# Performance work log

Hardware: AMD Instinct MI355X
Metric: run time of the kernel (lower is better)

The kernel has to match this reference:

```python
import jax, jax.numpy as jnp
import numpy as np

N_HEADS = 16
N_KV_HEADS = 4
ROPE_BASE = 10000.0


def rotate_half(x):
    d = x.shape[-1] // 2
    return jnp.concatenate((-x[..., d:], x[..., :d]), axis=-1)


def rope_cos_sin(seq_len, head_dim, dtype):
    inv_freq = 1.0 / (ROPE_BASE ** (jnp.arange(0, head_dim, 2, dtype=jnp.float32) / head_dim))
    t = jnp.arange(seq_len, dtype=jnp.float32)
    freqs = jnp.outer(t, inv_freq)            # [S, d/2]
    emb = jnp.concatenate((freqs, freqs), axis=-1)  # [S, d]
    return emb.astype(dtype), None  # placeholder; cos/sin computed by caller


def setup_inputs() -> dict:
    key = jax.random.key(0)
    ks = jax.random.split(key, 5)
    B, S, H = 1, 2048, 2048
    kv_dim = (H // N_HEADS) * N_KV_HEADS  # 512
    scale = 1.0 / np.sqrt(H)
    return {
        "hidden_states": jax.random.normal(ks[0], (B, S, H), dtype=jnp.float32),
        "Wq": jax.random.normal(ks[1], (H, H), dtype=jnp.float32) * scale,
        "Wk": jax.random.normal(ks[2], (kv_dim, H), dtype=jnp.float32) * scale,
        "Wv": jax.random.normal(ks[3], (kv_dim, H), dtype=jnp.float32) * scale,
        "Wo": jax.random.normal(ks[4], (H, H), dtype=jnp.float32) * scale,
    }


def reference(hidden_states, Wq, Wk, Wv, Wo):
    B, S, H = hidden_states.shape
    nH, nKV = N_HEADS, N_KV_HEADS
    d = H // nH
    groups = nH // nKV

    # projections (nn.Linear: y = x @ W.T)
    q = (hidden_states @ Wq.T).reshape(B, S, nH, d)   # [B,S,nH,d]
    k = (hidden_states @ Wk.T).reshape(B, S, nKV, d)  # [B,S,nKV,d]
    v = (hidden_states @ Wv.T).reshape(B, S, nKV, d)

    # RoPE
    inv_freq = 1.0 / (ROPE_BASE ** (jnp.arange(0, d, 2, dtype=jnp.float32) / d))
    freqs = jnp.outer(jnp.arange(S, dtype=jnp.float32), inv_freq)  # [S,d/2]
    emb = jnp.concatenate((freqs, freqs), axis=-1)                 # [S,d]
    cos = jnp.cos(emb)[None, :, None, :]
    sin = jnp.sin(emb)[None, :, None, :]
    q = q * cos + rotate_half(q) * sin
    k = k * cos + rotate_half(k) * sin

    # GQA: repeat_interleave kv heads over head axis
    k = jnp.repeat(k, groups, axis=2)  # [B,S,nH,d]
    v = jnp.repeat(v, groups, axis=2)

    # causal scaled dot-product attention
    scores = jnp.einsum('bqhd,bkhd->bhqk', q, k) / jnp.sqrt(jnp.asarray(d, q.dtype))
    causal = jnp.tril(jnp.ones((S, S), dtype=bool))
    scores = jnp.where(causal[None, None], scores, jnp.asarray(-jnp.inf, scores.dtype))
    probs = jax.nn.softmax(scores, axis=-1)
    out = jnp.einsum('bhqk,bkhd->bqhd', probs, v)  # [B,S,nH,d]
    out = out.reshape(B, S, H) @ Wo.T
    return out
```

## Files before the change

kernel.cpp:

```cpp
#include <hip/hip_runtime.h>
#include <cstdint>
#include <cstddef>


typedef __bf16 bf16_t;
typedef bf16_t bf16x4_t __attribute__((ext_vector_type(4)));
typedef bf16_t bf16x8_t __attribute__((ext_vector_type(8)));
typedef float f32x4_t __attribute__((ext_vector_type(4)));

__device__ __forceinline__ void async_copy16(void* lds_base, const void* gsrc) {
  auto g = reinterpret_cast<__attribute__((address_space(1))) void*>(
      reinterpret_cast<uintptr_t>(gsrc));
  auto l = reinterpret_cast<__attribute__((address_space(3))) void*>(
      static_cast<uint32_t>(reinterpret_cast<uintptr_t>(lds_base)));
  __builtin_amdgcn_global_load_lds(g, l, 16, 0, 0);
}

__global__ __launch_bounds__(256) void cvt_all(const float* __restrict__ hs,
                                               const float* __restrict__ wq,
                                               const float* __restrict__ wk,
                                               const float* __restrict__ wv,
                                               const float* __restrict__ wo,
                                               bf16_t* __restrict__ regA,
                                               bf16_t* __restrict__ regB,
                                               bf16_t* __restrict__ regWo) {
  const int b = blockIdx.x;
  const float* src;
  bf16_t* dst;
  int rel;
  if (b < 4096) { src = hs; dst = regA; rel = b; }
  else if (b < 8192) { src = wq; dst = regB; rel = b - 4096; }
  else if (b < 9216) { src = wk; dst = regB + 4194304; rel = b - 8192; }
  else if (b < 10240) { src = wv; dst = regB + 5242880; rel = b - 9216; }
  else { src = wo; dst = regWo; rel = b - 10240; }
  const int i = (rel * 256 + threadIdx.x) * 4;
  float4 v = *(const float4*)(src + i);
  bf16x4_t o = {(bf16_t)v.x, (bf16_t)v.y, (bf16_t)v.z, (bf16_t)v.w};
  *(bf16x4_t*)(dst + i) = o;
}

template <typename OutT, bool ROPE>
__global__ __launch_bounds__(256) void gemm_bt64(const bf16_t* __restrict__ A,
                                                 const bf16_t* __restrict__ B,
                                                 OutT* __restrict__ C,
                                                 int M, int N, int K) {
  __shared__ bf16_t As[64 * 64];
  __shared__ bf16_t Bs[128 * 64];
  const int tid = threadIdx.x;
  const int lane = tid & 63;
  const int quad = lane >> 4;
  const int l15 = lane & 15;
  const int l7 = l15 & 7;
  const int wave = tid >> 6;
  const int bm = blockIdx.x * 64;
  const int bn = blockIdx.y * 128;
  const int wm = (wave >> 1) * 32;
  const int wn32 = (wave & 1) * 32;
  const int coff[4] = {wn32, wn32 + 16, wn32 + 64, wn32 + 80};

  f32x4_t acc[2][4] = {};

  for (int k0 = 0; k0 < K; k0 += 64) {
#pragma unroll
    for (int it = 0; it < 2; ++it) {
      const int slot = it * 256 + tid;
      const int r = slot >> 3;
      const int q = (slot & 7) ^ (r & 7);
      const int wbase = it * 2048 + (tid & 192) * 8;
      async_copy16(As + wbase, A + (size_t)(bm + r) * K + k0 + q * 8);
    }
#pragma unroll
    for (int it = 0; it < 4; ++it) {
      const int slot = it * 256 + tid;
      const int r = slot >> 3;
      const int q = (slot & 7) ^ (r & 7);
      const int wbase = it * 2048 + (tid & 192) * 8;
      async_copy16(Bs + wbase, B + (size_t)(bn + r) * K + k0 + q * 8);
    }
    __syncthreads();
#pragma unroll
    for (int kk = 0; kk < 64; kk += 32) {
      const int kc = kk >> 3;
      bf16x8_t af[2], bfv[4];
#pragma unroll
      for (int i = 0; i < 2; ++i)
        af[i] = *(const bf16x8_t*)(As + (wm + i * 16 + l15) * 64 +
                                   (((kc + quad) ^ l7) * 8));
#pragma unroll
      for (int i = 0; i < 4; ++i)
        bfv[i] = *(const bf16x8_t*)(Bs + (coff[i] + l15) * 64 +
                                    (((kc + quad) ^ l7) * 8));
#pragma unroll
      for (int mi = 0; mi < 2; ++mi)
#pragma unroll
        for (int ni = 0; ni < 4; ++ni)
          acc[mi][ni] = __builtin_amdgcn_mfma_f32_16x16x32_bf16(
              af[mi], bfv[ni], acc[mi][ni], 0, 0, 0);
    }
    __syncthreads();
  }

  if (ROPE && bn < 2560) {
#pragma unroll
    for (int pair = 0; pair < 2; ++pair) {
      const int i_d = wn32 + pair * 16 + l15;
      const float inv = exp2f(-(float)i_d * 0.20762050593045702f);
#pragma unroll
      for (int mi = 0; mi < 2; ++mi) {
#pragma unroll
        for (int r = 0; r < 4; ++r) {
          const int s_row = bm + wm + mi * 16 + quad * 4 + r;
          float sn, cs;
          sincosf((float)s_row * inv, &sn, &cs);
          const float x0 = acc[mi][pair][r];
          const float x1 = acc[mi][pair + 2][r];
          acc[mi][pair][r] = x0 * cs - x1 * sn;
          acc[mi][pair + 2][r] = x1 * cs + x0 * sn;
        }
      }
    }
  }

#pragma unroll
  for (int mi = 0; mi < 2; ++mi) {
#pragma unroll
    for (int r = 0; r < 4; ++r) {
      const int row = bm + wm + mi * 16 + quad * 4 + r;
#pragma unroll
      for (int ni = 0; ni < 4; ++ni)
        C[(size_t)row * N + bn + coff[ni] + l15] = (OutT)acc[mi][ni][r];
    }
  }
}

__global__ __launch_bounds__(256) void attn_kernel(
    const bf16_t* __restrict__ qkv, float* __restrict__ Op,
    float* __restrict__ lp) {
  __shared__ bf16_t Ks[64 * 128];
  __shared__ bf16_t Vt[128 * 64];
  __shared__ bf16_t Ps[4 * 16 * 64];
  const int tid = threadIdx.x;
  const int lane = tid & 63;
  const int wave = tid >> 6;
  const int quad = lane >> 4;
  const int l15 = lane & 15;
  const int l7 = l15 & 7;
  const int j = blockIdx.x;
  const int half = j >> 9;
  const int j2 = j & 511;
  const int qb = (j2 < 256) ? (31 - (j2 >> 4)) : ((j2 - 256) >> 4);
  const int h = j2 & 15;
  const int kvh = h >> 2;
  const int nh0 = (qb + 2) >> 1;
  const int kbS = half ? nh0 : 0;
  const int kbE = half ? (qb + 1) : nh0;
  const float scale = 0.08838834764831845f;

  const int rk0 = tid >> 4;
  const int cq = tid & 15;
  const int dv2 = lane * 2;

  bf16x8_t qf[4];
  {
    const bf16_t* qbase =
        qkv + (size_t)(qb * 64 + wave * 16 + l15) * 3072 + h * 128 + quad * 8;
#pragma unroll
    for (int kf = 0; kf < 4; ++kf) qf[kf] = *(const bf16x8_t*)(qbase + kf * 32);
  }

  f32x4_t o[8] = {};
  float lsum[4] = {0.f, 0.f, 0.f, 0.f};

  bf16x8_t kreg[4];
  uint32_t vbuf[2][8];
  auto load_tile = [&](int kb) {
    const bf16_t* kbase = qkv + (size_t)(kb * 64) * 3072 + 2048 + kvh * 128;
    const bf16_t* vbase = qkv + (size_t)(kb * 64) * 3072 + 2560 + kvh * 128;
#pragma unroll
    for (int it = 0; it < 4; ++it)
      kreg[it] =
          *(const bf16x8_t*)(kbase + (size_t)(it * 16 + rk0) * 3072 + cq * 8);
#pragma unroll
    for (int it = 0; it < 2; ++it) {
      const int kg8 = it * 4 + wave;
#pragma unroll
      for (int t = 0; t < 8; ++t)
        vbuf[it][t] =
            *(const uint32_t*)(vbase + (size_t)(kg8 * 8 + t) * 3072 + dv2);
    }
  };

  if (kbS < kbE) {
    load_tile(kbS);

    for (int kb = kbS; kb < kbE; ++kb) {
      __syncthreads();
#pragma unroll
      for (int it = 0; it < 4; ++it)
        *(bf16x8_t*)(Ks + (it * 16 + rk0) * 128 + ((cq ^ rk0) * 8)) = kreg[it];
#pragma unroll
      for (int it = 0; it < 2; ++it) {
        const int kg8 = it * 4 + wave;
        bf16x8_t lov, hiv;
#pragma unroll
        for (int t = 0; t < 8; ++t) {
          const uint32_t u = vbuf[it][t];
          lov[t] = __builtin_bit_cast(bf16_t, (unsigned short)(u & 0xffff));
          hiv[t] = __builtin_bit_cast(bf16_t, (unsigned short)(u >> 16));
        }
        *(bf16x8_t*)(Vt + (size_t)dv2 * 64 + ((kg8 ^ (dv2 & 7)) * 8)) = lov;
        *(bf16x8_t*)(Vt + (size_t)(dv2 + 1) * 64 +
                     ((kg8 ^ ((dv2 + 1) & 7)) * 8)) = hiv;
      }
      __syncthreads();
      if (kb + 1 < kbE) load_tile(kb + 1);

      f32x4_t sc[4] = {};
#pragma unroll
      for (int kf = 0; kf < 4; ++kf) {
#pragma unroll
        for (int ni = 0; ni < 4; ++ni) {
          bf16x8_t bfr = *(const bf16x8_t*)(Ks + (ni * 16 + l15) * 128 +
                                            (((kf * 4 + quad) ^ l15) * 8));
          sc[ni] = __builtin_amdgcn_mfma_f32_16x16x32_bf16(qf[kf], bfr, sc[ni],
                                                           0, 0, 0);
        }
      }

      float p[4][4];
#pragma unroll
      for (int r = 0; r < 4; ++r) {
        const int sq = qb * 64 + wave * 16 + quad * 4 + r;
#pragma unroll
        for (int ni = 0; ni < 4; ++ni) {
          float arg = fmaf(sc[ni][r], scale, -16.0f);
          if (kb == qb && (kb * 64 + ni * 16 + l15) > sq) arg = -100.0f;
          const float e = __expf(arg);
          p[ni][r] = e;
          lsum[r] += e;
        }
      }

      bf16_t* pw = Ps + wave * 16 * 64;
#pragma unroll
      for (int ni = 0; ni < 4; ++ni)
#pragma unroll
        for (int r = 0; r < 4; ++r) {
          const int prow = quad * 4 + r;
          pw[prow * 64 + (((ni * 2 + (l15 >> 3)) ^ (prow & 7)) * 8) + l7] =
              (bf16_t)p[ni][r];
        }

#pragma unroll
      for (int kf = 0; kf < 2; ++kf) {
        bf16x8_t af =
            *(const bf16x8_t*)(pw + l15 * 64 + (((kf * 4 + quad) ^ l7) * 8));
#pragma unroll
        for (int ni = 0; ni < 8; ++ni) {
          bf16x8_t bfr = *(const bf16x8_t*)(Vt + (ni * 16 + l15) * 64 +
                                            (((kf * 4 + quad) ^ l7) * 8));
          o[ni] =
              __builtin_amdgcn_mfma_f32_16x16x32_bf16(af, bfr, o[ni], 0, 0, 0);
        }
      }
    }
  }

#pragma unroll
  for (int m = 1; m <= 8; m <<= 1)
#pragma unroll
    for (int r = 0; r < 4; ++r) lsum[r] += __shfl_xor(lsum[r], m, 64);

  float* obase = Op + (size_t)half * 4194304 +
                 (size_t)(qb * 64 + wave * 16 + quad * 4) * 2048 + h * 128 + l15;
#pragma unroll
  for (int r = 0; r < 4; ++r) {
#pragma unroll
    for (int ni = 0; ni < 8; ++ni)
      obase[(size_t)r * 2048 + ni * 16] = o[ni][r];
    if (l15 == 0) {
      const int row = qb * 64 + wave * 16 + quad * 4 + r;
      lp[(half * 2048 + row) * 16 + h] = lsum[r];
    }
  }
}

__global__ __launch_bounds__(256) void combine_kernel(
    const float* __restrict__ Op, const float* __restrict__ lp,
    bf16_t* __restrict__ out) {
  const int idx = (blockIdx.x * 256 + threadIdx.x) * 4;
  const int s = idx >> 11;
  const int col = idx & 2047;
  const int h = col >> 7;
  const float l = lp[s * 16 + h] + lp[(2048 + s) * 16 + h];
  const float inv = 1.0f / l;
  float4 a = *(const float4*)(Op + (size_t)s * 2048 + col);
  float4 b = *(const float4*)(Op + 4194304 + (size_t)s * 2048 + col);
  bf16x4_t o = {(bf16_t)((a.x + b.x) * inv), (bf16_t)((a.y + b.y) * inv),
                (bf16_t)((a.z + b.z) * inv), (bf16_t)((a.w + b.w) * inv)};
  *(bf16x4_t*)(out + idx) = o;
}

extern "C" void kernel_launch(void* const* d_in, const int* in_sizes, int n_in,
                              void* d_out, int out_size, void* d_ws, size_t ws_size,
                              hipStream_t stream) {
  const float* hidden = (const float*)d_in[0];
  const float* Wq = (const float*)d_in[1];
  const float* Wk = (const float*)d_in[2];
  const float* Wv = (const float*)d_in[3];
  const float* Wo = (const float*)d_in[4];

  char* ws = (char*)d_ws;
  bf16_t* regA = (bf16_t*)ws;
  bf16_t* regB = (bf16_t*)(ws + (size_t)(8u << 20));
  float* Opart = (float*)(ws + (size_t)(8u << 20));
  bf16_t* regC = (bf16_t*)(ws + (size_t)(40u << 20));
  bf16_t* regWo = (bf16_t*)(ws + (size_t)(53u << 20));
  float* lpart = (float*)(ws + (size_t)(61u << 20));

  cvt_all<<<14336, 256, 0, stream>>>(hidden, Wq, Wk, Wv, Wo, regA, regB, regWo);

  gemm_bt64<bf16_t, true><<<dim3(32, 24), 256, 0, stream>>>(regA, regB, regC,
                                                            2048, 3072, 2048);

  attn_kernel<<<1024, 256, 0, stream>>>(regC, Opart, lpart);

  combine_kernel<<<4096, 256, 0, stream>>>(Opart, lpart, regA);

  gemm_bt64<float, false><<<dim3(32, 16), 256, 0, stream>>>(
      regA, regWo, (float*)d_out, 2048, 2048, 2048);
}
```

Measured before the change: 217.4 us.

## Double attention query tile per block to reuse K/V tiles across two row groups

Each attention block now handles 128 query rows (32 per wave, as two 16-row MFMA groups) instead of 64, so every K/V tile loaded into LDS feeds twice as many MFMAs. The grid drops from 1024 to 512 blocks, and the causal split into two halves is recomputed over 64-wide key tiles with a new mask condition. This cuts global K/V traffic and LDS staging per unit of work, at the cost of more registers per thread (doubled accumulators and Q fragments), a larger P buffer, and fewer blocks to keep the GPU occupied.

```diff
diff --git a/kernel.cpp b/kernel.cpp
--- a/kernel.cpp
+++ b/kernel.cpp
@@ -138,7 +138,7 @@
     float* __restrict__ lp) {
   __shared__ bf16_t Ks[64 * 128];
   __shared__ bf16_t Vt[128 * 64];
-  __shared__ bf16_t Ps[4 * 16 * 64];
+  __shared__ bf16_t Ps[4 * 32 * 64];
   const int tid = threadIdx.x;
   const int lane = tid & 63;
   const int wave = tid >> 6;
@@ -146,30 +146,32 @@
   const int l15 = lane & 15;
   const int l7 = l15 & 7;
   const int j = blockIdx.x;
-  const int half = j >> 9;
-  const int j2 = j & 511;
-  const int qb = (j2 < 256) ? (31 - (j2 >> 4)) : ((j2 - 256) >> 4);
-  const int h = j2 & 15;
+  const int half = (j >= 256);
+  const int qb = half ? ((j - 256) >> 4) : (15 - (j >> 4));
+  const int h = j & 15;
   const int kvh = h >> 2;
-  const int nh0 = (qb + 2) >> 1;
-  const int kbS = half ? nh0 : 0;
-  const int kbE = half ? (qb + 1) : nh0;
+  const int nt = 2 * qb + 2;
+  const int kbS = half ? (qb + 1) : 0;
+  const int kbE = half ? nt : (qb + 1);
   const float scale = 0.08838834764831845f;
 
   const int rk0 = tid >> 4;
   const int cq = tid & 15;
   const int dv2 = lane * 2;
 
-  bf16x8_t qf[4];
-  {
+  bf16x8_t qf[2][4];
+#pragma unroll
+  for (int g = 0; g < 2; ++g) {
     const bf16_t* qbase =
-        qkv + (size_t)(qb * 64 + wave * 16 + l15) * 3072 + h * 128 + quad * 8;
-#pragma unroll
-    for (int kf = 0; kf < 4; ++kf) qf[kf] = *(const bf16x8_t*)(qbase + kf * 32);
-  }
-
-  f32x4_t o[8] = {};
-  float lsum[4] = {0.f, 0.f, 0.f, 0.f};
+        qkv + (size_t)(qb * 128 + wave * 32 + g * 16 + l15) * 3072 + h * 128 +
+        quad * 8;
+#pragma unroll
+    for (int kf = 0; kf < 4; ++kf)
+      qf[g][kf] = *(const bf16x8_t*)(qbase + kf * 32);
+  }
+
+  f32x4_t o[2][8] = {};
+  float lsum[2][4] = {};
 
   bf16x8_t kreg[4];
   uint32_t vbuf[2][8];
@@ -190,78 +192,87 @@
     }
   };
 
-  if (kbS < kbE) {
-    load_tile(kbS);
-
-    for (int kb = kbS; kb < kbE; ++kb) {
-      __syncthreads();
-#pragma unroll
-      for (int it = 0; it < 4; ++it)
-        *(bf16x8_t*)(Ks + (it * 16 + rk0) * 128 + ((cq ^ rk0) * 8)) = kreg[it];
-#pragma unroll
-      for (int it = 0; it < 2; ++it) {
-        const int kg8 = it * 4 + wave;
-        bf16x8_t lov, hiv;
-#pragma unroll
-        for (int t = 0; t < 8; ++t) {
-          const uint32_t u = vbuf[it][t];
-          lov[t] = __builtin_bit_cast(bf16_t, (unsigned short)(u & 0xffff));
-          hiv[t] = __builtin_bit_cast(bf16_t, (unsigned short)(u >> 16));
-        }
-        *(bf16x8_t*)(Vt + (size_t)dv2 * 64 + ((kg8 ^ (dv2 & 7)) * 8)) = lov;
-        *(bf16x8_t*)(Vt + (size_t)(dv2 + 1) * 64 +
-                     ((kg8 ^ ((dv2 + 1) & 7)) * 8)) = hiv;
-      }
-      __syncthreads();
-      if (kb + 1 < kbE) load_tile(kb + 1);
-
-      f32x4_t sc[4] = {};
-#pragma unroll
-      for (int kf = 0; kf < 4; ++kf) {
+  load_tile(kbS);
+
+  for (int kb = kbS; kb < kbE; ++kb) {
+    __syncthreads();
+#pragma unroll
+    for (int it = 0; it < 4; ++it)
+      *(bf16x8_t*)(Ks + (it * 16 + rk0) * 128 + ((cq ^ rk0) * 8)) = kreg[it];
+#pragma unroll
+    for (int it = 0; it < 2; ++it) {
+      const int kg8 = it * 4 + wave;
+      bf16x8_t lov, hiv;
+#pragma unroll
+      for (int t = 0; t < 8; ++t) {
+        const uint32_t u = vbuf[it][t];
+        lov[t] = __builtin_bit_cast(bf16_t, (unsigned short)(u & 0xffff));
+        hiv[t] = __builtin_bit_cast(bf16_t, (unsigned short)(u >> 16));
+      }
+      *(bf16x8_t*)(Vt + (size_t)dv2 * 64 + ((kg8 ^ (dv2 & 7)) * 8)) = lov;
+      *(bf16x8_t*)(Vt + (size_t)(dv2 + 1) * 64 +
+                   ((kg8 ^ ((dv2 + 1) & 7)) * 8)) = hiv;
+    }
+    __syncthreads();
+    if (kb + 1 < kbE) load_tile(kb + 1);
+
+    f32x4_t sc[2][4] = {};
+#pragma unroll
+    for (int kf = 0; kf < 4; ++kf) {
+#pragma unroll
+      for (int ni = 0; ni < 4; ++ni) {
+        bf16x8_t bfr = *(const bf16x8_t*)(Ks + (ni * 16 + l15) * 128 +
+                                          (((kf * 4 + quad) ^ l15) * 8));
+#pragma unroll
+        for (int g = 0; g < 2; ++g)
+          sc[g][ni] = __builtin_amdgcn_mfma_f32_16x16x32_bf16(
+              qf[g][kf], bfr, sc[g][ni], 0, 0, 0);
+      }
+    }
+
+    const bool need_mask = (kb >= 2 * qb);
+#pragma unroll
+    for (int g = 0; g < 2; ++g) {
+      float p[4][4];
+#pragma unroll
+      for (int r = 0; r < 4; ++r) {
+        const int sq = qb * 128 + wave * 32 + g * 16 + quad * 4 + r;
 #pragma unroll
         for (int ni = 0; ni < 4; ++ni) {
-          bf16x8_t bfr = *(const bf16x8_t*)(Ks + (ni * 16 + l15) * 128 +
-                                            (((kf * 4 + quad) ^ l15) * 8));
-          sc[ni] = __builtin_amdgcn_mfma_f32_16x16x32_bf16(qf[kf], bfr, sc[ni],
-                                                           0, 0, 0);
-        }
-      }
-
-      float p[4][4];
-#pragma unroll
-      for (int r = 0; r < 4; ++r) {
-        const int sq = qb * 64 + wave * 16 + quad * 4 + r;
-#pragma unroll
-        for (int ni = 0; ni < 4; ++ni) {
-          float arg = fmaf(sc[ni][r], scale, -16.0f);
-          if (kb == qb && (kb * 64 + ni * 16 + l15) > sq) arg = -100.0f;
+          float arg = fmaf(sc[g][ni][r], scale, -16.0f);
+          if (need_mask && (kb * 64 + ni * 16 + l15) > sq) arg = -100.0f;
           const float e = __expf(arg);
           p[ni][r] = e;
-          lsum[r] += e;
+          lsum[g][r] += e;
         }
       }
-
-      bf16_t* pw = Ps + wave * 16 * 64;
+      bf16_t* pw = Ps + wave * 32 * 64;
 #pragma unroll
       for (int ni = 0; ni < 4; ++ni)
 #pragma unroll
         for (int r = 0; r < 4; ++r) {
-          const int prow = quad * 4 + r;
+          const int prow = g * 16 + quad * 4 + r;
           pw[prow * 64 + (((ni * 2 + (l15 >> 3)) ^ (prow & 7)) * 8) + l7] =
               (bf16_t)p[ni][r];
         }
-
-#pragma unroll
-      for (int kf = 0; kf < 2; ++kf) {
-        bf16x8_t af =
-            *(const bf16x8_t*)(pw + l15 * 64 + (((kf * 4 + quad) ^ l7) * 8));
-#pragma unroll
-        for (int ni = 0; ni < 8; ++ni) {
-          bf16x8_t bfr = *(const bf16x8_t*)(Vt + (ni * 16 + l15) * 64 +
-                                            (((kf * 4 + quad) ^ l7) * 8));
-          o[ni] =
-              __builtin_amdgcn_mfma_f32_16x16x32_bf16(af, bfr, o[ni], 0, 0, 0);
-        }
+    }
+
+    bf16_t* pw = Ps + wave * 32 * 64;
+#pragma unroll
+    for (int kf = 0; kf < 2; ++kf) {
+      bf16x8_t af[2];
+#pragma unroll
+      for (int g = 0; g < 2; ++g)
+        af[g] = *(const bf16x8_t*)(pw + (g * 16 + l15) * 64 +
+                                   (((kf * 4 + quad) ^ l7) * 8));
+#pragma unroll
+      for (int ni = 0; ni < 8; ++ni) {
+        bf16x8_t bfr = *(const bf16x8_t*)(Vt + (ni * 16 + l15) * 64 +
+                                          (((kf * 4 + quad) ^ l7) * 8));
+#pragma unroll
+        for (int g = 0; g < 2; ++g)
+          o[g][ni] = __builtin_amdgcn_mfma_f32_16x16x32_bf16(af[g], bfr,
+                                                             o[g][ni], 0, 0, 0);
       }
     }
   }
@@ -269,18 +280,21 @@
 #pragma unroll
   for (int m = 1; m <= 8; m <<= 1)
 #pragma unroll
-    for (int r = 0; r < 4; ++r) lsum[r] += __shfl_xor(lsum[r], m, 64);
-
-  float* obase = Op + (size_t)half * 4194304 +
-                 (size_t)(qb * 64 + wave * 16 + quad * 4) * 2048 + h * 128 + l15;
-#pragma unroll
-  for (int r = 0; r < 4; ++r) {
-#pragma unroll
-    for (int ni = 0; ni < 8; ++ni)
-      obase[(size_t)r * 2048 + ni * 16] = o[ni][r];
-    if (l15 == 0) {
-      const int row = qb * 64 + wave * 16 + quad * 4 + r;
-      lp[(half * 2048 + row) * 16 + h] = lsum[r];
+    for (int g = 0; g < 2; ++g)
+#pragma unroll
+      for (int r = 0; r < 4; ++r) lsum[g][r] += __shfl_xor(lsum[g][r], m, 64);
+
+#pragma unroll
+  for (int g = 0; g < 2; ++g) {
+    const int row0 = qb * 128 + wave * 32 + g * 16 + quad * 4;
+    float* obase = Op + (size_t)half * 4194304 + (size_t)row0 * 2048 +
+                   h * 128 + l15;
+#pragma unroll
+    for (int r = 0; r < 4; ++r) {
+#pragma unroll
+      for (int ni = 0; ni < 8; ++ni)
+        obase[(size_t)r * 2048 + ni * 16] = o[g][ni][r];
+      if (l15 == 0) lp[(half * 2048 + row0 + r) * 16 + h] = lsum[g][r];
     }
   }
 }
@@ -323,7 +337,7 @@
   gemm_bt64<bf16_t, true><<<dim3(32, 24), 256, 0, stream>>>(regA, regB, regC,
                                                             2048, 3072, 2048);
 
-  attn_kernel<<<1024, 256, 0, stream>>>(regC, Opart, lpart);
+  attn_kernel<<<512, 256, 0, stream>>>(regC, Opart, lpart);
 
   combine_kernel<<<4096, 256, 0, stream>>>(Opart, lpart, regA);
 
```

New measurement: 249.3 us. 1.15x slower.
